# Performance work log

Hardware: AMD Instinct MI355X
Metric: run time of the kernel (lower is better)

The kernel has to match this reference:

```python
import jax, jax.numpy as jnp
import numpy as np

B, Q, LE, D, P, A = 8, 32, 128, 512, 32, 128


def setup_inputs() -> dict:
    key = jax.random.key(0)
    ks = jax.random.split(key, 8)
    exp_tokens = jax.random.normal(ks[0], (B, Q, LE, D), dtype=jnp.float32)
    exp_mask = jax.random.randint(ks[1], (B, Q, LE), 0, 2, dtype=jnp.int32)
    s_j = jax.random.normal(ks[2], (B, P, D), dtype=jnp.float32)
    req_mask = jax.random.randint(ks[3], (B, P), 0, 2, dtype=jnp.int32)
    sc = 1.0 / np.sqrt(D)
    Ws_w = jax.random.normal(ks[4], (A, D), dtype=jnp.float32) * sc
    Ws_b = jax.random.normal(ks[5], (A,), dtype=jnp.float32) * 0.01
    U_w = jax.random.normal(ks[6], (A, D), dtype=jnp.float32) * sc
    v_w = jax.random.normal(ks[7], (1, A), dtype=jnp.float32) * (1.0 / np.sqrt(A))
    return {"exp_tokens": exp_tokens, "exp_mask": exp_mask, "s_j": s_j,
            "req_mask": req_mask, "Ws_w": Ws_w, "Ws_b": Ws_b, "U_w": U_w, "v_w": v_w}


def reference(exp_tokens, exp_mask, s_j, req_mask, Ws_w, Ws_b, U_w, v_w):
    # ws: (B,P,A); uh: (B,Q,Le,A)
    ws = jnp.einsum('bpd,ad->bpa', s_j, Ws_w) + Ws_b
    uh = jnp.einsum('bqtd,ad->bqta', exp_tokens, U_w)
    # broadcast add -> (B,Q,P,Le,A), tanh, project with v -> (B,Q,P,Le)
    scored = jnp.tanh(uh[:, :, None, :, :] + ws[:, None, :, None, :])
    e = jnp.einsum('bqpta,a->bqpt', scored, v_w[0])
    tok_mask = exp_mask[:, :, None, :]  # (B,Q,1,Le) broadcast over P
    e = jnp.where(tok_mask == 0, jnp.float32(-1e9), e)
    # joint softmax over Q*Le per (b,p)
    e_t = jnp.transpose(e, (0, 2, 1, 3)).reshape(e.shape[0], e.shape[2], -1)
    a = jax.nn.softmax(e_t, axis=-1).reshape(e.shape[0], e.shape[2], e.shape[1], e.shape[3])
    a = jnp.transpose(a, (0, 2, 1, 3))  # (B,Q,P,Le)
    s_rlk = jnp.einsum('bqpt,bqtd->bqpd', a, exp_tokens)
    rmask = req_mask[:, None, :, None].astype(s_rlk.dtype)
    return s_rlk * rmask
```

## Files before the change

### kernel.cpp

```cpp
#include <hip/hip_runtime.h>
#include <hip/hip_bf16.h>

#define B_  8
#define Q_  32
#define LE_ 128
#define D_  512
#define P_  32
#define A_  128

typedef __attribute__((ext_vector_type(8))) short short8_t;
typedef __attribute__((ext_vector_type(4))) float floatx4_t;
typedef float f32x2 __attribute__((ext_vector_type(2)));

typedef const __attribute__((address_space(1))) unsigned int glb_uint;
typedef __attribute__((address_space(3))) unsigned int lds_uint;
#define GLD16(g, s) __builtin_amdgcn_global_load_lds((glb_uint*)(g), (lds_uint*)(s), 16, 0, 0)

__device__ __forceinline__ short f2bf(float x) {
    unsigned u = __float_as_uint(x);
    unsigned r = (u + 0x7fffu + ((u >> 16) & 1u)) >> 16;
    return (short)r;
}

__global__ __launch_bounds__(256) void convert_kernel(
    const float* __restrict__ X, const float* __restrict__ W,
    short* __restrict__ Xb, short* __restrict__ Wb) {
    int b = blockIdx.x;
    const float* src;
    short* dst;
    size_t base;
    if (b < 8192) {
        base = ((size_t)b * 256 + threadIdx.x) * 8;
        src = X + base; dst = Xb + base;
    } else {
        base = ((size_t)(b - 8192) * 256 + threadIdx.x) * 8;
        src = W + base; dst = Wb + base;
    }
    float4 v0 = ((const float4*)src)[0];
    float4 v1 = ((const float4*)src)[1];
    short8_t s;
    s[0] = f2bf(v0.x); s[1] = f2bf(v0.y); s[2] = f2bf(v0.z); s[3] = f2bf(v0.w);
    s[4] = f2bf(v1.x); s[5] = f2bf(v1.y); s[6] = f2bf(v1.z); s[7] = f2bf(v1.w);
    *(short8_t*)dst = s;
}

__global__ __launch_bounds__(128) void ws_kernel(
    const float* __restrict__ s_j, const float* __restrict__ Ws_w,
    const float* __restrict__ Ws_b, float* __restrict__ ws) {
    __shared__ float s_row[D_];
    int bp = blockIdx.x;
    const float* src = s_j + (size_t)bp * D_;
    for (int i = threadIdx.x; i < D_; i += 128) s_row[i] = src[i];
    __syncthreads();
    int a = threadIdx.x;
    const float4* w4 = (const float4*)(Ws_w + (size_t)a * D_);
    const float4* s4 = (const float4*)s_row;
    float acc = 0.0f;
#pragma unroll 8
    for (int i = 0; i < D_ / 4; ++i) {
        float4 w = w4[i];
        float4 s = s4[i];
        acc += w.x * s.x + w.y * s.y + w.z * s.z + w.w * s.w;
    }
    ws[bp * A_ + a] = __expf(2.0f * (acc + Ws_b[a]));
}

__global__ __launch_bounds__(256, 2) void uh_mfma_kernel(
    const short* __restrict__ Xb, const short* __restrict__ Wb,
    float* __restrict__ uh) {
    __shared__ short As[64 * 64];
    __shared__ short Bs[128 * 64];
    int mblk = blockIdx.x * 64;
    int tid = threadIdx.x;
    int wave = tid >> 6, lane = tid & 63;
    int qd = lane >> 4, lr = lane & 15;
    int mh = wave >> 1, nh = wave & 1;
    int axor = lr & 7;

    int cA = lane & 7;
    int rowA0 = wave * 16 + (lane >> 3);
    int rowB0 = wave * 32 + (lane >> 3);

    floatx4_t acc[2][4];
#pragma unroll
    for (int i = 0; i < 2; ++i)
#pragma unroll
        for (int j = 0; j < 4; ++j) acc[i][j] = (floatx4_t){0.f, 0.f, 0.f, 0.f};

    for (int kt = 0; kt < 8; ++kt) {
        int k0 = kt * 64;
        if (kt) __syncthreads();
#pragma unroll
        for (int u = 0; u < 2; ++u) {
            int m = rowA0 + u * 8;
            const short* g = Xb + (size_t)(mblk + m) * D_ + k0 + ((cA ^ (m & 7)) * 8);
            GLD16(g, As + (wave * 2 + u) * 512);
        }
#pragma unroll
        for (int u = 0; u < 4; ++u) {
            int n = rowB0 + u * 8;
            const short* g = Wb + (size_t)n * D_ + k0 + ((cA ^ (n & 7)) * 8);
            GLD16(g, Bs + (wave * 4 + u) * 512);
        }
        __syncthreads();
#pragma unroll
        for (int ks = 0; ks < 2; ++ks) {
            int cr = (ks * 4 + qd) ^ axor;
            short8_t af[2], bfr[4];
#pragma unroll
            for (int i = 0; i < 2; ++i)
                af[i] = *(const short8_t*)(As + (mh * 32 + i * 16 + lr) * 64 + cr * 8);
#pragma unroll
            for (int j = 0; j < 4; ++j)
                bfr[j] = *(const short8_t*)(Bs + (nh * 64 + j * 16 + lr) * 64 + cr * 8);
#pragma unroll
            for (int i = 0; i < 2; ++i)
#pragma unroll
                for (int j = 0; j < 4; ++j)
                    acc[i][j] = __builtin_amdgcn_mfma_f32_16x16x32_bf16(af[i], bfr[j], acc[i][j], 0, 0, 0);
        }
    }
#pragma unroll
    for (int i = 0; i < 2; ++i) {
#pragma unroll
        for (int j = 0; j < 4; ++j) {
            int mg = mblk + mh * 32 + i * 16 + qd * 4;
            int ng = nh * 64 + j * 16 + lr;
            float* dst = uh + (size_t)mg * A_ + ng;
#pragma unroll
            for (int r = 0; r < 4; ++r)
                dst[(size_t)r * A_] = __expf(2.0f * acc[i][j][r]);
        }
    }
}

__global__ __launch_bounds__(256) void score_kernel(
    const float* __restrict__ EU, const float* __restrict__ EW,
    const float* __restrict__ v_w, const int* __restrict__ exp_mask,
    float* __restrict__ Ee) {
    __shared__ float eu_t[32][132];
    __shared__ float ew_t[32][128];
    __shared__ float n2v[128];
    int blk = blockIdx.x;
    int bq = blk >> 2, tc = blk & 3;
    int b = bq >> 5;
    int t0 = tc * 32;
    int tid = threadIdx.x;

#pragma unroll
    for (int i = 0; i < 4; ++i) {
        int f = tid + i * 256;
        int t = f >> 5, a4 = f & 31;
        float4 v = *(const float4*)(EU + (size_t)(bq * LE_ + t0 + t) * A_ + a4 * 4);
        *(float4*)&eu_t[t][a4 * 4] = v;
    }
#pragma unroll
    for (int i = 0; i < 4; ++i) {
        int f = tid + i * 256;
        int p = f >> 5, a4 = f & 31;
        *(float4*)&ew_t[p][a4 * 4] =
            *(const float4*)(EW + (size_t)(b * P_ + p) * A_ + a4 * 4);
    }
    if (tid < 32) {
        float4 v = *(const float4*)(v_w + tid * 4);
        v.x *= -2.0f; v.y *= -2.0f; v.z *= -2.0f; v.w *= -2.0f;
        *(float4*)&n2v[tid * 4] = v;
    }
    __syncthreads();

    int t = tid & 31, pb = tid >> 5;
    int mask = exp_mask[bq * LE_ + t0 + t];
    float acc[4] = {0.f, 0.f, 0.f, 0.f};
    for (int a4 = 0; a4 < 32; ++a4) {
        float4 u = *(const float4*)&eu_t[t][a4 * 4];
        float4 vv = *(const float4*)&n2v[a4 * 4];
#pragma unroll
        for (int i = 0; i < 4; ++i) {
            float4 w = *(const float4*)&ew_t[pb + i * 8][a4 * 4];
            acc[i] = fmaf(vv.x, __builtin_amdgcn_rcpf(fmaf(u.x, w.x, 1.0f)), acc[i]);
            acc[i] = fmaf(vv.y, __builtin_amdgcn_rcpf(fmaf(u.y, w.y, 1.0f)), acc[i]);
            acc[i] = fmaf(vv.z, __builtin_amdgcn_rcpf(fmaf(u.z, w.z, 1.0f)), acc[i]);
            acc[i] = fmaf(vv.w, __builtin_amdgcn_rcpf(fmaf(u.w, w.w, 1.0f)), acc[i]);
        }
    }
#pragma unroll
    for (int i = 0; i < 4; ++i) {
        int p = pb + i * 8;
        Ee[(size_t)(bq * P_ + p) * LE_ + t0 + t] = mask ? __expf(acc[i]) : 0.0f;
    }
}

__global__ __launch_bounds__(256) void softmax_stats_kernel(
    const float* __restrict__ Ee, float* __restrict__ rinv) {
    __shared__ float red[4];
    int bp = blockIdx.x;
    int b = bp >> 5, p = bp & 31;
    int tid = threadIdx.x;
    float s = 0.0f;
#pragma unroll
    for (int i = 0; i < 16; ++i) {
        int idx = tid + i * 256;
        int q = idx >> 7, t = idx & 127;
        s += Ee[(size_t)((b * Q_ + q) * P_ + p) * LE_ + t];
    }
    for (int off = 32; off; off >>= 1) s += __shfl_down(s, off);
    int wid = tid >> 6;
    if ((tid & 63) == 0) red[wid] = s;
    __syncthreads();
    if (tid == 0)
        rinv[bp] = 1.0f / (red[0] + red[1] + red[2] + red[3]);
}

#define WSTRIDE 20
__global__ __launch_bounds__(256) void out_kernel(
    const float* __restrict__ Ee, const float* __restrict__ rinv,
    const short* __restrict__ Xb, const int* __restrict__ req_mask,
    float* __restrict__ out) {
    __shared__ float w_s[LE_ * WSTRIDE];
    int bq = blockIdx.x >> 1, ph = blockIdx.x & 1;
    int b = bq >> 5;
    int p0 = ph * 16;
    int tid = threadIdx.x;

#pragma unroll
    for (int i = 0; i < 8; ++i) {
        int idx = tid + i * 256;
        int t = idx & 127, p = idx >> 7;
        int bp = b * P_ + p0 + p;
        float rm = req_mask[bp] ? rinv[bp] : 0.0f;
        w_s[t * WSTRIDE + p] = Ee[(size_t)(bq * P_ + p0 + p) * LE_ + t] * rm;
    }
    __syncthreads();

    const unsigned* Tb = (const unsigned*)(Xb + (size_t)bq * LE_ * D_);
    f32x2 acc2[16];
#pragma unroll
    for (int p = 0; p < 16; ++p) acc2[p] = (f32x2){0.f, 0.f};

#pragma unroll 4
    for (int t = 0; t < LE_; ++t) {
        unsigned uv = Tb[t * (D_ / 2) + tid];
        f32x2 tv = (f32x2){__uint_as_float(uv << 16),
                           __uint_as_float(uv & 0xffff0000u)};
        const float4* wp = (const float4*)&w_s[t * WSTRIDE];
#pragma unroll
        for (int j = 0; j < 4; ++j) {
            float4 w = wp[j];
            acc2[j * 4 + 0] = (f32x2){w.x, w.x} * tv + acc2[j * 4 + 0];
            acc2[j * 4 + 1] = (f32x2){w.y, w.y} * tv + acc2[j * 4 + 1];
            acc2[j * 4 + 2] = (f32x2){w.z, w.z} * tv + acc2[j * 4 + 2];
            acc2[j * 4 + 3] = (f32x2){w.w, w.w} * tv + acc2[j * 4 + 3];
        }
    }
    float* obase = out + (size_t)(bq * P_ + p0) * D_ + tid * 2;
#pragma unroll
    for (int p = 0; p < 16; ++p)
        *(float2*)(obase + (size_t)p * D_) = make_float2(acc2[p].x, acc2[p].y);
}

extern "C" void kernel_launch(void* const* d_in, const int* in_sizes, int n_in,
                              void* d_out, int out_size, void* d_ws, size_t ws_size,
                              hipStream_t stream) {
    const float* exp_tokens = (const float*)d_in[0];
    const int*   exp_mask   = (const int*)d_in[1];
    const float* s_j        = (const float*)d_in[2];
    const int*   req_mask   = (const int*)d_in[3];
    const float* Ws_w       = (const float*)d_in[4];
    const float* Ws_b       = (const float*)d_in[5];
    const float* U_w        = (const float*)d_in[6];
    const float* v_w        = (const float*)d_in[7];
    float* out = (float*)d_out;

    float* ws_buf = (float*)d_ws;
    float* uh     = ws_buf + B_ * P_ * A_;
    float* Ee     = uh + (size_t)B_ * Q_ * LE_ * A_;
    float* rinv   = Ee + (size_t)B_ * Q_ * P_ * LE_;
    short* Xb     = (short*)(rinv + 256);
    short* Wb     = Xb + (size_t)B_ * Q_ * LE_ * D_;

    convert_kernel<<<dim3(8192 + 32), dim3(256), 0, stream>>>(exp_tokens, U_w, Xb, Wb);
    ws_kernel<<<dim3(B_ * P_), dim3(128), 0, stream>>>(s_j, Ws_w, Ws_b, ws_buf);
    uh_mfma_kernel<<<dim3(B_ * Q_ * LE_ / 64), dim3(256), 0, stream>>>(Xb, Wb, uh);
    score_kernel<<<dim3(B_ * Q_ * 4), dim3(256), 0, stream>>>(uh, ws_buf, v_w, exp_mask, Ee);
    softmax_stats_kernel<<<dim3(B_ * P_), dim3(256), 0, stream>>>(Ee, rinv);
    out_kernel<<<dim3(B_ * Q_ * 2), dim3(256), 0, stream>>>(Ee, rinv, Xb, req_mask, out);
}
```

Before: 183.1 us.

## Use MFMA for output contraction with bf16 weights and fused softmax sums

```diff
diff --git a/kernel.cpp b/kernel.cpp
--- a/kernel.cpp
+++ b/kernel.cpp
@@ -22,26 +22,43 @@
     return (short)r;
 }
 
+#define TP_ 136
 __global__ __launch_bounds__(256) void convert_kernel(
     const float* __restrict__ X, const float* __restrict__ W,
-    short* __restrict__ Xb, short* __restrict__ Wb) {
-    int b = blockIdx.x;
-    const float* src;
-    short* dst;
-    size_t base;
-    if (b < 8192) {
-        base = ((size_t)b * 256 + threadIdx.x) * 8;
-        src = X + base; dst = Xb + base;
-    } else {
-        base = ((size_t)(b - 8192) * 256 + threadIdx.x) * 8;
-        src = W + base; dst = Wb + base;
-    }
-    float4 v0 = ((const float4*)src)[0];
-    float4 v1 = ((const float4*)src)[1];
-    short8_t s;
-    s[0] = f2bf(v0.x); s[1] = f2bf(v0.y); s[2] = f2bf(v0.z); s[3] = f2bf(v0.w);
-    s[4] = f2bf(v1.x); s[5] = f2bf(v1.y); s[6] = f2bf(v1.z); s[7] = f2bf(v1.w);
-    *(short8_t*)dst = s;
+    short* __restrict__ Xb, short* __restrict__ XbT, short* __restrict__ Wb) {
+    int blk = blockIdx.x;
+    int tid = threadIdx.x;
+    if (blk >= 1024) {
+        size_t base = (size_t)(blk - 1024) * 2048 + tid * 8;
+        float4 v0 = ((const float4*)(W + base))[0];
+        float4 v1 = ((const float4*)(W + base))[1];
+        short8_t s;
+        s[0] = f2bf(v0.x); s[1] = f2bf(v0.y); s[2] = f2bf(v0.z); s[3] = f2bf(v0.w);
+        s[4] = f2bf(v1.x); s[5] = f2bf(v1.y); s[6] = f2bf(v1.z); s[7] = f2bf(v1.w);
+        *(short8_t*)(Wb + base) = s;
+        return;
+    }
+    __shared__ short tile[128 * TP_];
+    int bq = blk >> 2, d0 = (blk & 3) * 128;
+    int tt = tid >> 5, dd = (tid & 31) * 4;
+#pragma unroll 4
+    for (int pass = 0; pass < 16; ++pass) {
+        int t = tt + pass * 8;
+        float4 v = *(const float4*)(X + (size_t)(bq * LE_ + t) * D_ + d0 + dd);
+        short s0 = f2bf(v.x), s1 = f2bf(v.y), s2 = f2bf(v.z), s3 = f2bf(v.w);
+        short* xd = Xb + (size_t)(bq * LE_ + t) * D_ + d0 + dd;
+        xd[0] = s0; xd[1] = s1; xd[2] = s2; xd[3] = s3;
+        tile[(dd + 0) * TP_ + t] = s0;
+        tile[(dd + 1) * TP_ + t] = s1;
+        tile[(dd + 2) * TP_ + t] = s2;
+        tile[(dd + 3) * TP_ + t] = s3;
+    }
+    __syncthreads();
+    int dr = tid >> 1, th = (tid & 1) * 64;
+    short* dst = XbT + ((size_t)(bq * D_) + d0 + dr) * LE_ + th;
+#pragma unroll
+    for (int i = 0; i < 8; ++i)
+        *(short8_t*)(dst + i * 8) = *(const short8_t*)(tile + dr * TP_ + th + i * 8);
 }
 
 __global__ __launch_bounds__(128) void ws_kernel(
@@ -137,7 +154,7 @@
 __global__ __launch_bounds__(256) void score_kernel(
     const float* __restrict__ EU, const float* __restrict__ EW,
     const float* __restrict__ v_w, const int* __restrict__ exp_mask,
-    float* __restrict__ Ee) {
+    short* __restrict__ Eeb, float* __restrict__ sums) {
     __shared__ float eu_t[32][132];
     __shared__ float ew_t[32][128];
     __shared__ float n2v[128];
@@ -186,76 +203,83 @@
 #pragma unroll
     for (int i = 0; i < 4; ++i) {
         int p = pb + i * 8;
-        Ee[(size_t)(bq * P_ + p) * LE_ + t0 + t] = mask ? __expf(acc[i]) : 0.0f;
-    }
-}
-
-__global__ __launch_bounds__(256) void softmax_stats_kernel(
-    const float* __restrict__ Ee, float* __restrict__ rinv) {
-    __shared__ float red[4];
-    int bp = blockIdx.x;
-    int b = bp >> 5, p = bp & 31;
+        float ev = mask ? __expf(acc[i]) : 0.0f;
+        Eeb[(size_t)(bq * P_ + p) * LE_ + t0 + t] = f2bf(ev);
+        float s = ev;
+        s += __shfl_down(s, 16, 32);
+        s += __shfl_down(s, 8, 32);
+        s += __shfl_down(s, 4, 32);
+        s += __shfl_down(s, 2, 32);
+        s += __shfl_down(s, 1, 32);
+        if (t == 0) atomicAdd(&sums[b * P_ + p], s);
+    }
+}
+
+#define WP_ 140
+__global__ __launch_bounds__(256) void out_mfma_kernel(
+    const short* __restrict__ Eeb, const float* __restrict__ sums,
+    const short* __restrict__ XbT, const int* __restrict__ req_mask,
+    float* __restrict__ out) {
+    __shared__ short wlds[32 * WP_];
+    __shared__ float rinv_s[32];
+    int bq = blockIdx.x >> 2, dq = blockIdx.x & 3;
+    int b = bq >> 5;
     int tid = threadIdx.x;
-    float s = 0.0f;
-#pragma unroll
-    for (int i = 0; i < 16; ++i) {
-        int idx = tid + i * 256;
-        int q = idx >> 7, t = idx & 127;
-        s += Ee[(size_t)((b * Q_ + q) * P_ + p) * LE_ + t];
-    }
-    for (int off = 32; off; off >>= 1) s += __shfl_down(s, off);
-    int wid = tid >> 6;
-    if ((tid & 63) == 0) red[wid] = s;
+
+#pragma unroll
+    for (int i = 0; i < 2; ++i) {
+        int c = tid + i * 256;
+        int p = c >> 4, off = (c & 15) * 8;
+        short8_t v = *(const short8_t*)(Eeb + ((size_t)bq * P_ + p) * LE_ + off);
+        *(short8_t*)(wlds + p * WP_ + off) = v;
+    }
+    if (tid < 32) {
+        int bp = b * P_ + tid;
+        float s = sums[bp];
+        rinv_s[tid] = req_mask[bp] ? __fdividef(1.0f, s) : 0.0f;
+    }
     __syncthreads();
-    if (tid == 0)
-        rinv[bp] = 1.0f / (red[0] + red[1] + red[2] + red[3]);
-}
-
-#define WSTRIDE 20
-__global__ __launch_bounds__(256) void out_kernel(
-    const float* __restrict__ Ee, const float* __restrict__ rinv,
-    const short* __restrict__ Xb, const int* __restrict__ req_mask,
-    float* __restrict__ out) {
-    __shared__ float w_s[LE_ * WSTRIDE];
-    int bq = blockIdx.x >> 1, ph = blockIdx.x & 1;
-    int b = bq >> 5;
-    int p0 = ph * 16;
-    int tid = threadIdx.x;
-
-#pragma unroll
-    for (int i = 0; i < 8; ++i) {
-        int idx = tid + i * 256;
-        int t = idx & 127, p = idx >> 7;
-        int bp = b * P_ + p0 + p;
-        float rm = req_mask[bp] ? rinv[bp] : 0.0f;
-        w_s[t * WSTRIDE + p] = Ee[(size_t)(bq * P_ + p0 + p) * LE_ + t] * rm;
-    }
-    __syncthreads();
-
-    const unsigned* Tb = (const unsigned*)(Xb + (size_t)bq * LE_ * D_);
-    f32x2 acc2[16];
-#pragma unroll
-    for (int p = 0; p < 16; ++p) acc2[p] = (f32x2){0.f, 0.f};
-
-#pragma unroll 4
-    for (int t = 0; t < LE_; ++t) {
-        unsigned uv = Tb[t * (D_ / 2) + tid];
-        f32x2 tv = (f32x2){__uint_as_float(uv << 16),
-                           __uint_as_float(uv & 0xffff0000u)};
-        const float4* wp = (const float4*)&w_s[t * WSTRIDE];
-#pragma unroll
-        for (int j = 0; j < 4; ++j) {
-            float4 w = wp[j];
-            acc2[j * 4 + 0] = (f32x2){w.x, w.x} * tv + acc2[j * 4 + 0];
-            acc2[j * 4 + 1] = (f32x2){w.y, w.y} * tv + acc2[j * 4 + 1];
-            acc2[j * 4 + 2] = (f32x2){w.z, w.z} * tv + acc2[j * 4 + 2];
-            acc2[j * 4 + 3] = (f32x2){w.w, w.w} * tv + acc2[j * 4 + 3];
-        }
-    }
-    float* obase = out + (size_t)(bq * P_ + p0) * D_ + tid * 2;
-#pragma unroll
-    for (int p = 0; p < 16; ++p)
-        *(float2*)(obase + (size_t)p * D_) = make_float2(acc2[p].x, acc2[p].y);
+
+    int wave = tid >> 6, lane = tid & 63;
+    int qd = lane >> 4, lr = lane & 15;
+    int n0 = dq * 128 + wave * 32;
+
+    short8_t af[2][4];
+#pragma unroll
+    for (int i = 0; i < 2; ++i)
+#pragma unroll
+        for (int ks = 0; ks < 4; ++ks)
+            af[i][ks] = *(const short8_t*)(wlds + (i * 16 + lr) * WP_ + ks * 32 + qd * 8);
+
+    floatx4_t acc[2][2];
+#pragma unroll
+    for (int i = 0; i < 2; ++i)
+#pragma unroll
+        for (int j = 0; j < 2; ++j) acc[i][j] = (floatx4_t){0.f, 0.f, 0.f, 0.f};
+
+    const short* Bbase = XbT + (size_t)bq * D_ * LE_;
+#pragma unroll
+    for (int ks = 0; ks < 4; ++ks) {
+#pragma unroll
+        for (int j = 0; j < 2; ++j) {
+            short8_t bfr = *(const short8_t*)(Bbase + (size_t)(n0 + j * 16 + lr) * LE_ + ks * 32 + qd * 8);
+            acc[0][j] = __builtin_amdgcn_mfma_f32_16x16x32_bf16(af[0][ks], bfr, acc[0][j], 0, 0, 0);
+            acc[1][j] = __builtin_amdgcn_mfma_f32_16x16x32_bf16(af[1][ks], bfr, acc[1][j], 0, 0, 0);
+        }
+    }
+#pragma unroll
+    for (int i = 0; i < 2; ++i) {
+#pragma unroll
+        for (int r = 0; r < 4; ++r) {
+            int p = i * 16 + qd * 4 + r;
+            float rm = rinv_s[p];
+#pragma unroll
+            for (int j = 0; j < 2; ++j) {
+                int d = n0 + j * 16 + lr;
+                out[((size_t)bq * P_ + p) * D_ + d] = acc[i][j][r] * rm;
+            }
+        }
+    }
 }
 
 extern "C" void kernel_launch(void* const* d_in, const int* in_sizes, int n_in,
@@ -271,17 +295,18 @@
     const float* v_w        = (const float*)d_in[7];
     float* out = (float*)d_out;
 
-    float* ws_buf = (float*)d_ws;
-    float* uh     = ws_buf + B_ * P_ * A_;
-    float* Ee     = uh + (size_t)B_ * Q_ * LE_ * A_;
-    float* rinv   = Ee + (size_t)B_ * Q_ * P_ * LE_;
-    short* Xb     = (short*)(rinv + 256);
-    short* Wb     = Xb + (size_t)B_ * Q_ * LE_ * D_;
-
-    convert_kernel<<<dim3(8192 + 32), dim3(256), 0, stream>>>(exp_tokens, U_w, Xb, Wb);
-    ws_kernel<<<dim3(B_ * P_), dim3(128), 0, stream>>>(s_j, Ws_w, Ws_b, ws_buf);
-    uh_mfma_kernel<<<dim3(B_ * Q_ * LE_ / 64), dim3(256), 0, stream>>>(Xb, Wb, uh);
-    score_kernel<<<dim3(B_ * Q_ * 4), dim3(256), 0, stream>>>(uh, ws_buf, v_w, exp_mask, Ee);
-    softmax_stats_kernel<<<dim3(B_ * P_), dim3(256), 0, stream>>>(Ee, rinv);
-    out_kernel<<<dim3(B_ * Q_ * 2), dim3(256), 0, stream>>>(Ee, rinv, Xb, req_mask, out);
-}
+    float* EW   = (float*)d_ws;
+    float* EU   = EW + B_ * P_ * A_;
+    float* sums = EU + (size_t)B_ * Q_ * LE_ * A_;
+    short* Eeb  = (short*)(sums + 256);
+    short* Xb   = Eeb + (size_t)B_ * Q_ * P_ * LE_;
+    short* XbT  = Xb + (size_t)B_ * Q_ * LE_ * D_;
+    short* Wb   = XbT + (size_t)B_ * Q_ * LE_ * D_;
+
+    hipMemsetAsync(sums, 0, B_ * P_ * sizeof(float), stream);
+    convert_kernel<<<dim3(1024 + 32), dim3(256), 0, stream>>>(exp_tokens, U_w, Xb, XbT, Wb);
+    ws_kernel<<<dim3(B_ * P_), dim3(128), 0, stream>>>(s_j, Ws_w, Ws_b, EW);
+    uh_mfma_kernel<<<dim3(B_ * Q_ * LE_ / 64), dim3(256), 0, stream>>>(Xb, Wb, EU);
+    score_kernel<<<dim3(B_ * Q_ * 4), dim3(256), 0, stream>>>(EU, EW, v_w, exp_mask, Eeb, sums);
+    out_mfma_kernel<<<dim3(B_ * Q_ * 4), dim3(256), 0, stream>>>(Eeb, sums, XbT, req_mask, out);
+}
```

After: 208.3 us. +13.8%, slower.

## Fuse uh GEMM, scoring, softmax sums and output GEMM into one per-bq kernel

Applied to the files above, without the earlier changes.

```diff
diff --git a/kernel.cpp b/kernel.cpp
--- a/kernel.cpp
+++ b/kernel.cpp
@@ -10,7 +10,6 @@
 
 typedef __attribute__((ext_vector_type(8))) short short8_t;
 typedef __attribute__((ext_vector_type(4))) float floatx4_t;
-typedef float f32x2 __attribute__((ext_vector_type(2)));
 
 typedef const __attribute__((address_space(1))) unsigned int glb_uint;
 typedef __attribute__((address_space(3))) unsigned int lds_uint;
@@ -20,6 +19,9 @@
     unsigned u = __float_as_uint(x);
     unsigned r = (u + 0x7fffu + ((u >> 16) & 1u)) >> 16;
     return (short)r;
+}
+__device__ __forceinline__ float bf2f(short s) {
+    return __uint_as_float(((unsigned)(unsigned short)s) << 16);
 }
 
 __global__ __launch_bounds__(256) void convert_kernel(
@@ -65,21 +67,33 @@
     ws[bp * A_ + a] = __expf(2.0f * (acc + Ws_b[a]));
 }
 
-__global__ __launch_bounds__(256, 2) void uh_mfma_kernel(
+#define EUP_ 136
+#define EWP_ 132
+#define WPP_ 136
+
+__global__ __launch_bounds__(512, 1) void fused_kernel(
     const short* __restrict__ Xb, const short* __restrict__ Wb,
-    float* __restrict__ uh) {
-    __shared__ short As[64 * 64];
-    __shared__ short Bs[128 * 64];
-    int mblk = blockIdx.x * 64;
+    const float* __restrict__ EW, const float* __restrict__ v_w,
+    const int* __restrict__ exp_mask, float* __restrict__ gsums,
+    float* __restrict__ out) {
+    __shared__ short uA[128 * EUP_];
+    __shared__ float ew_s[32 * EWP_];
+    __shared__ short w_s[32 * WPP_];
+    __shared__ float n2v[128];
+    __shared__ int   mask_s[128];
+
+    int bq = blockIdx.x;
+    int b  = bq >> 5;
     int tid = threadIdx.x;
     int wave = tid >> 6, lane = tid & 63;
     int qd = lane >> 4, lr = lane & 15;
-    int mh = wave >> 1, nh = wave & 1;
-    int axor = lr & 7;
-
+
+    short* As = uA;
+    short* Bs = uA + 8192;
+
+    int m0 = (wave >> 1) * 32, n0 = (wave & 1) * 64;
     int cA = lane & 7;
-    int rowA0 = wave * 16 + (lane >> 3);
-    int rowB0 = wave * 32 + (lane >> 3);
+    int row0 = wave * 16 + (lane >> 3);
 
     floatx4_t acc[2][4];
 #pragma unroll
@@ -89,30 +103,30 @@
 
     for (int kt = 0; kt < 8; ++kt) {
         int k0 = kt * 64;
-        if (kt) __syncthreads();
+        __syncthreads();
 #pragma unroll
         for (int u = 0; u < 2; ++u) {
-            int m = rowA0 + u * 8;
-            const short* g = Xb + (size_t)(mblk + m) * D_ + k0 + ((cA ^ (m & 7)) * 8);
-            GLD16(g, As + (wave * 2 + u) * 512);
-        }
-#pragma unroll
-        for (int u = 0; u < 4; ++u) {
-            int n = rowB0 + u * 8;
-            const short* g = Wb + (size_t)n * D_ + k0 + ((cA ^ (n & 7)) * 8);
-            GLD16(g, Bs + (wave * 4 + u) * 512);
+            int m = row0 + u * 8;
+            GLD16(Xb + (size_t)(bq * 128 + m) * D_ + k0 + ((cA ^ (m & 7)) * 8),
+                  As + (wave * 2 + u) * 512);
+        }
+#pragma unroll
+        for (int u = 0; u < 2; ++u) {
+            int n = row0 + u * 8;
+            GLD16(Wb + (size_t)n * D_ + k0 + ((cA ^ (n & 7)) * 8),
+                  Bs + (wave * 2 + u) * 512);
         }
         __syncthreads();
 #pragma unroll
         for (int ks = 0; ks < 2; ++ks) {
-            int cr = (ks * 4 + qd) ^ axor;
+            int cr = (ks * 4 + qd) ^ (lr & 7);
             short8_t af[2], bfr[4];
 #pragma unroll
             for (int i = 0; i < 2; ++i)
-                af[i] = *(const short8_t*)(As + (mh * 32 + i * 16 + lr) * 64 + cr * 8);
+                af[i] = *(const short8_t*)(As + (m0 + i * 16 + lr) * 64 + cr * 8);
 #pragma unroll
             for (int j = 0; j < 4; ++j)
-                bfr[j] = *(const short8_t*)(Bs + (nh * 64 + j * 16 + lr) * 64 + cr * 8);
+                bfr[j] = *(const short8_t*)(Bs + (n0 + j * 16 + lr) * 64 + cr * 8);
 #pragma unroll
             for (int i = 0; i < 2; ++i)
 #pragma unroll
@@ -120,142 +134,131 @@
                     acc[i][j] = __builtin_amdgcn_mfma_f32_16x16x32_bf16(af[i], bfr[j], acc[i][j], 0, 0, 0);
         }
     }
-#pragma unroll
-    for (int i = 0; i < 2; ++i) {
-#pragma unroll
-        for (int j = 0; j < 4; ++j) {
-            int mg = mblk + mh * 32 + i * 16 + qd * 4;
-            int ng = nh * 64 + j * 16 + lr;
-            float* dst = uh + (size_t)mg * A_ + ng;
-#pragma unroll
-            for (int r = 0; r < 4; ++r)
-                dst[(size_t)r * A_] = __expf(2.0f * acc[i][j][r]);
-        }
-    }
-}
-
-__global__ __launch_bounds__(256) void score_kernel(
-    const float* __restrict__ EU, const float* __restrict__ EW,
-    const float* __restrict__ v_w, const int* __restrict__ exp_mask,
-    float* __restrict__ Ee) {
-    __shared__ float eu_t[32][132];
-    __shared__ float ew_t[32][128];
-    __shared__ float n2v[128];
-    int blk = blockIdx.x;
-    int bq = blk >> 2, tc = blk & 3;
-    int b = bq >> 5;
-    int t0 = tc * 32;
-    int tid = threadIdx.x;
-
-#pragma unroll
-    for (int i = 0; i < 4; ++i) {
-        int f = tid + i * 256;
-        int t = f >> 5, a4 = f & 31;
-        float4 v = *(const float4*)(EU + (size_t)(bq * LE_ + t0 + t) * A_ + a4 * 4);
-        *(float4*)&eu_t[t][a4 * 4] = v;
-    }
-#pragma unroll
-    for (int i = 0; i < 4; ++i) {
-        int f = tid + i * 256;
-        int p = f >> 5, a4 = f & 31;
-        *(float4*)&ew_t[p][a4 * 4] =
-            *(const float4*)(EW + (size_t)(b * P_ + p) * A_ + a4 * 4);
+    __syncthreads();
+
+#pragma unroll
+    for (int i = 0; i < 2; ++i)
+#pragma unroll
+        for (int j = 0; j < 4; ++j)
+#pragma unroll
+            for (int r = 0; r < 4; ++r) {
+                int t = m0 + i * 16 + qd * 4 + r;
+                int a = n0 + j * 16 + lr;
+                uA[t * EUP_ + a] = f2bf(__expf(2.0f * acc[i][j][r]));
+            }
+#pragma unroll
+    for (int u = 0; u < 2; ++u) {
+        int c = tid * 2 + u;
+        int p = c >> 5, seg = c & 31;
+        *(float4*)&ew_s[p * EWP_ + seg * 4] =
+            *(const float4*)&EW[(size_t)(b * P_ + p) * A_ + seg * 4];
     }
     if (tid < 32) {
         float4 v = *(const float4*)(v_w + tid * 4);
         v.x *= -2.0f; v.y *= -2.0f; v.z *= -2.0f; v.w *= -2.0f;
         *(float4*)&n2v[tid * 4] = v;
     }
-    __syncthreads();
-
-    int t = tid & 31, pb = tid >> 5;
-    int mask = exp_mask[bq * LE_ + t0 + t];
-    float acc[4] = {0.f, 0.f, 0.f, 0.f};
-    for (int a4 = 0; a4 < 32; ++a4) {
-        float4 u = *(const float4*)&eu_t[t][a4 * 4];
-        float4 vv = *(const float4*)&n2v[a4 * 4];
-#pragma unroll
-        for (int i = 0; i < 4; ++i) {
-            float4 w = *(const float4*)&ew_t[pb + i * 8][a4 * 4];
-            acc[i] = fmaf(vv.x, __builtin_amdgcn_rcpf(fmaf(u.x, w.x, 1.0f)), acc[i]);
-            acc[i] = fmaf(vv.y, __builtin_amdgcn_rcpf(fmaf(u.y, w.y, 1.0f)), acc[i]);
-            acc[i] = fmaf(vv.z, __builtin_amdgcn_rcpf(fmaf(u.z, w.z, 1.0f)), acc[i]);
-            acc[i] = fmaf(vv.w, __builtin_amdgcn_rcpf(fmaf(u.w, w.w, 1.0f)), acc[i]);
-        }
-    }
-#pragma unroll
-    for (int i = 0; i < 4; ++i) {
-        int p = pb + i * 8;
-        Ee[(size_t)(bq * P_ + p) * LE_ + t0 + t] = mask ? __expf(acc[i]) : 0.0f;
-    }
-}
-
-__global__ __launch_bounds__(256) void softmax_stats_kernel(
-    const float* __restrict__ Ee, float* __restrict__ rinv) {
-    __shared__ float red[4];
-    int bp = blockIdx.x;
-    int b = bp >> 5, p = bp & 31;
-    int tid = threadIdx.x;
-    float s = 0.0f;
-#pragma unroll
-    for (int i = 0; i < 16; ++i) {
-        int idx = tid + i * 256;
-        int q = idx >> 7, t = idx & 127;
-        s += Ee[(size_t)((b * Q_ + q) * P_ + p) * LE_ + t];
-    }
-    for (int off = 32; off; off >>= 1) s += __shfl_down(s, off);
-    int wid = tid >> 6;
-    if ((tid & 63) == 0) red[wid] = s;
-    __syncthreads();
-    if (tid == 0)
-        rinv[bp] = 1.0f / (red[0] + red[1] + red[2] + red[3]);
-}
-
-#define WSTRIDE 20
-__global__ __launch_bounds__(256) void out_kernel(
-    const float* __restrict__ Ee, const float* __restrict__ rinv,
-    const short* __restrict__ Xb, const int* __restrict__ req_mask,
-    float* __restrict__ out) {
-    __shared__ float w_s[LE_ * WSTRIDE];
-    int bq = blockIdx.x >> 1, ph = blockIdx.x & 1;
-    int b = bq >> 5;
-    int p0 = ph * 16;
-    int tid = threadIdx.x;
-
-#pragma unroll
-    for (int i = 0; i < 8; ++i) {
-        int idx = tid + i * 256;
-        int t = idx & 127, p = idx >> 7;
-        int bp = b * P_ + p0 + p;
-        float rm = req_mask[bp] ? rinv[bp] : 0.0f;
-        w_s[t * WSTRIDE + p] = Ee[(size_t)(bq * P_ + p0 + p) * LE_ + t] * rm;
-    }
-    __syncthreads();
-
-    const unsigned* Tb = (const unsigned*)(Xb + (size_t)bq * LE_ * D_);
-    f32x2 acc2[16];
-#pragma unroll
-    for (int p = 0; p < 16; ++p) acc2[p] = (f32x2){0.f, 0.f};
-
-#pragma unroll 4
-    for (int t = 0; t < LE_; ++t) {
-        unsigned uv = Tb[t * (D_ / 2) + tid];
-        f32x2 tv = (f32x2){__uint_as_float(uv << 16),
-                           __uint_as_float(uv & 0xffff0000u)};
-        const float4* wp = (const float4*)&w_s[t * WSTRIDE];
-#pragma unroll
-        for (int j = 0; j < 4; ++j) {
-            float4 w = wp[j];
-            acc2[j * 4 + 0] = (f32x2){w.x, w.x} * tv + acc2[j * 4 + 0];
-            acc2[j * 4 + 1] = (f32x2){w.y, w.y} * tv + acc2[j * 4 + 1];
-            acc2[j * 4 + 2] = (f32x2){w.z, w.z} * tv + acc2[j * 4 + 2];
-            acc2[j * 4 + 3] = (f32x2){w.w, w.w} * tv + acc2[j * 4 + 3];
-        }
-    }
-    float* obase = out + (size_t)(bq * P_ + p0) * D_ + tid * 2;
-#pragma unroll
-    for (int p = 0; p < 16; ++p)
-        *(float2*)(obase + (size_t)p * D_) = make_float2(acc2[p].x, acc2[p].y);
+    if (tid < 128) mask_s[tid] = exp_mask[bq * LE_ + tid];
+    __syncthreads();
+
+    {
+        int t = tid & 127, pg = tid >> 7;
+        float acc8[8];
+#pragma unroll
+        for (int j = 0; j < 8; ++j) acc8[j] = 0.0f;
+        for (int a8 = 0; a8 < 16; ++a8) {
+            short8_t e8 = *(const short8_t*)&uA[t * EUP_ + a8 * 8];
+            float eu[8];
+#pragma unroll
+            for (int k = 0; k < 8; ++k) eu[k] = bf2f(e8[k]);
+            float4 nv0 = *(const float4*)&n2v[a8 * 8];
+            float4 nv1 = *(const float4*)&n2v[a8 * 8 + 4];
+            float nv[8] = {nv0.x, nv0.y, nv0.z, nv0.w, nv1.x, nv1.y, nv1.z, nv1.w};
+#pragma unroll
+            for (int j = 0; j < 8; ++j) {
+                int p = pg * 8 + j;
+                float4 w0 = *(const float4*)&ew_s[p * EWP_ + a8 * 8];
+                float4 w1 = *(const float4*)&ew_s[p * EWP_ + a8 * 8 + 4];
+                float ww[8] = {w0.x, w0.y, w0.z, w0.w, w1.x, w1.y, w1.z, w1.w};
+#pragma unroll
+                for (int k = 0; k < 8; ++k)
+                    acc8[j] = fmaf(nv[k], __builtin_amdgcn_rcpf(fmaf(eu[k], ww[k], 1.0f)), acc8[j]);
+            }
+        }
+        int mk = mask_s[t];
+#pragma unroll
+        for (int j = 0; j < 8; ++j) {
+            float ee = mk ? __expf(acc8[j]) : 0.0f;
+            w_s[(pg * 8 + j) * WPP_ + t] = f2bf(ee);
+        }
+    }
+    __syncthreads();
+
+    if (tid < 256) {
+        int p = tid >> 3, seg = tid & 7;
+        const short* src = w_s + p * WPP_ + seg * 16;
+        float s = 0.0f;
+#pragma unroll
+        for (int k = 0; k < 16; ++k) s += bf2f(src[k]);
+        s += __shfl_xor(s, 1);
+        s += __shfl_xor(s, 2);
+        s += __shfl_xor(s, 4);
+        if (seg == 0) atomicAdd(&gsums[b * P_ + p], s);
+    }
+
+    short8_t afv[2][4];
+#pragma unroll
+    for (int i = 0; i < 2; ++i)
+#pragma unroll
+        for (int ks = 0; ks < 4; ++ks)
+            afv[i][ks] = *(const short8_t*)&w_s[(i * 16 + lr) * WPP_ + ks * 32 + qd * 8];
+
+    int tt = tid >> 2, dseg = (tid & 3) * 32;
+    for (int chunk = 0; chunk < 4; ++chunk) {
+        int d0 = chunk * 128;
+        __syncthreads();
+        const short8_t* g = (const short8_t*)(Xb + (size_t)(bq * 128 + tt) * D_ + d0 + dseg);
+        short8_t xs0 = g[0], xs1 = g[1], xs2 = g[2], xs3 = g[3];
+#pragma unroll
+        for (int e = 0; e < 8; ++e) {
+            uA[(dseg + 0 + e) * EUP_ + tt]  = xs0[e];
+            uA[(dseg + 8 + e) * EUP_ + tt]  = xs1[e];
+            uA[(dseg + 16 + e) * EUP_ + tt] = xs2[e];
+            uA[(dseg + 24 + e) * EUP_ + tt] = xs3[e];
+        }
+        __syncthreads();
+        floatx4_t accp[2];
+        accp[0] = (floatx4_t){0.f, 0.f, 0.f, 0.f};
+        accp[1] = (floatx4_t){0.f, 0.f, 0.f, 0.f};
+#pragma unroll
+        for (int ks = 0; ks < 4; ++ks) {
+            short8_t bfr = *(const short8_t*)&uA[(wave * 16 + lr) * EUP_ + ks * 32 + qd * 8];
+            accp[0] = __builtin_amdgcn_mfma_f32_16x16x32_bf16(afv[0][ks], bfr, accp[0], 0, 0, 0);
+            accp[1] = __builtin_amdgcn_mfma_f32_16x16x32_bf16(afv[1][ks], bfr, accp[1], 0, 0, 0);
+        }
+#pragma unroll
+        for (int i = 0; i < 2; ++i)
+#pragma unroll
+            for (int r = 0; r < 4; ++r) {
+                int p = i * 16 + qd * 4 + r;
+                out[((size_t)bq * P_ + p) * D_ + d0 + wave * 16 + lr] = accp[i][r];
+            }
+    }
+}
+
+__global__ __launch_bounds__(256) void norm_kernel(
+    float* __restrict__ out, const float* __restrict__ gsums,
+    const int* __restrict__ req_mask) {
+    int bqp = blockIdx.x;
+    int p = bqp & 31;
+    int b = bqp >> 10;
+    int bp = b * P_ + p;
+    float s = gsums[bp];
+    float rm = req_mask[bp] ? __fdividef(1.0f, s) : 0.0f;
+    float2* o = (float2*)(out + (size_t)bqp * D_);
+    float2 v = o[threadIdx.x];
+    v.x *= rm; v.y *= rm;
+    o[threadIdx.x] = v;
 }
 
 extern "C" void kernel_launch(void* const* d_in, const int* in_sizes, int n_in,
@@ -271,17 +274,14 @@
     const float* v_w        = (const float*)d_in[7];
     float* out = (float*)d_out;
 
-    float* ws_buf = (float*)d_ws;
-    float* uh     = ws_buf + B_ * P_ * A_;
-    float* Ee     = uh + (size_t)B_ * Q_ * LE_ * A_;
-    float* rinv   = Ee + (size_t)B_ * Q_ * P_ * LE_;
-    short* Xb     = (short*)(rinv + 256);
-    short* Wb     = Xb + (size_t)B_ * Q_ * LE_ * D_;
-
+    float* EW    = (float*)d_ws;
+    float* gsums = EW + B_ * P_ * A_;
+    short* Xb    = (short*)(gsums + 256);
+    short* Wb    = Xb + (size_t)B_ * Q_ * LE_ * D_;
+
+    hipMemsetAsync(gsums, 0, B_ * P_ * sizeof(float), stream);
     convert_kernel<<<dim3(8192 + 32), dim3(256), 0, stream>>>(exp_tokens, U_w, Xb, Wb);
-    ws_kernel<<<dim3(B_ * P_), dim3(128), 0, stream>>>(s_j, Ws_w, Ws_b, ws_buf);
-    uh_mfma_kernel<<<dim3(B_ * Q_ * LE_ / 64), dim3(256), 0, stream>>>(Xb, Wb, uh);
-    score_kernel<<<dim3(B_ * Q_ * 4), dim3(256), 0, stream>>>(uh, ws_buf, v_w, exp_mask, Ee);
-    softmax_stats_kernel<<<dim3(B_ * P_), dim3(256), 0, stream>>>(Ee, rinv);
-    out_kernel<<<dim3(B_ * Q_ * 2), dim3(256), 0, stream>>>(Ee, rinv, Xb, req_mask, out);
-}
+    ws_kernel<<<dim3(B_ * P_), dim3(128), 0, stream>>>(s_j, Ws_w, Ws_b, EW);
+    fused_kernel<<<dim3(B_ * Q_), dim3(512), 0, stream>>>(Xb, Wb, EW, v_w, exp_mask, gsums, out);
+    norm_kernel<<<dim3(B_ * Q_ * P_), dim3(256), 0, stream>>>(out, gsums, req_mask);
+}
```

Measured after the change: 169.6 us. -7.3%, faster.
